# Kernel optimization log

Hardware: AMD Instinct MI355X
Metric: run time of the kernel (lower is better)

The kernel has to match this reference:

```python
import jax, jax.numpy as jnp
import numpy as np

NEG_SLOPE = 0.2

def leaky_relu(x):
    return jnp.where(x >= 0, x, NEG_SLOPE * x)

def conv1x1(x, w, b):
    # x: [n,c,h,w], w: [o,c], b: [o]
    return jnp.einsum('nchw,oc->nohw', x, w) + b[None, :, None, None]

def setup_inputs() -> dict:
    key = jax.random.key(0)
    ks = jax.random.split(key, 7)
    n, c, h, w = 4, 64, 80, 80
    scale = 1.0 / np.sqrt(c)
    return {
        'x': jax.random.normal(ks[0], (n, c, h, w), dtype=jnp.float32),
        'w1': jax.random.normal(ks[1], (c, c), dtype=jnp.float32) * scale,
        'b1': jax.random.normal(ks[2], (c,), dtype=jnp.float32) * 0.01,
        'w2': jax.random.normal(ks[3], (c, c), dtype=jnp.float32) * scale,
        'b2': jax.random.normal(ks[4], (c,), dtype=jnp.float32) * 0.01,
        'w3': jax.random.normal(ks[5], (c, c), dtype=jnp.float32) * scale,
        'b3': jax.random.normal(ks[6], (c,), dtype=jnp.float32) * 0.01,
    }

def reference(x, w1, b1, w2, b2, w3, b3):
    n, c, h, w = x.shape
    e1 = leaky_relu(conv1x1(x, w1, b1))  # [n,c,h,w]
    e2 = leaky_relu(conv1x1(x, w2, b2))
    asm = leaky_relu(conv1x1(x, w3, b3))
    # q: [n, hw, c]; k: [n, c, hw]
    q = e1.transpose(0, 2, 3, 1).reshape(n, h * w, c)
    k = e2.reshape(n, c, h * w)
    score = jax.nn.softmax(jnp.matmul(q, k), axis=2)  # [n, hw, hw]
    v = asm.reshape(n, c, h * w).transpose(0, 2, 1)   # [n, hw, c]
    out = jnp.matmul(score, v)                        # [n, hw, c]
    return out.transpose(0, 2, 1).reshape(n, c, h, w)
```

## Files before the change

kernel.cpp:

```cpp
#include <hip/hip_runtime.h>


typedef __attribute__((ext_vector_type(8))) unsigned short us8;
typedef __attribute__((ext_vector_type(4))) unsigned short us4;
typedef __attribute__((ext_vector_type(8))) __bf16 bf16x8;
typedef __attribute__((ext_vector_type(16))) float f32x16;

#define HW 6400
#define L2E 1.44269504088896340736f
#define KS 5
#define ITERS 20

union V8 { us8 s; us4 h[2]; bf16x8 b; unsigned u4[4]; };

__device__ __forceinline__ unsigned short f32_to_bf16(float f) {
  unsigned u = __float_as_uint(f);
  u += 0x7fffu + ((u >> 16) & 1u);
  return (unsigned short)(u >> 16);
}
__device__ __forceinline__ float bf16_bits_to_f32(unsigned short u) {
  return __uint_as_float(((unsigned)u) << 16);
}
__device__ __forceinline__ unsigned pack_bf16x2(float a, float b) {
#if __has_builtin(__builtin_amdgcn_cvt_pk_bf16_f32)
  auto v = __builtin_amdgcn_cvt_pk_bf16_f32(a, b);
  unsigned u;
  __builtin_memcpy(&u, &v, 4);
  return u;
#else
  unsigned ua = __float_as_uint(a); ua += 0x7fffu + ((ua >> 16) & 1u);
  unsigned ub = __float_as_uint(b); ub += 0x7fffu + ((ub >> 16) & 1u);
  return (ua >> 16) | (ub & 0xffff0000u);
#endif
}

__device__ __forceinline__ void split_hilo(const float* f, V8& hi, V8& lo) {
#pragma unroll
  for (int j = 0; j < 8; ++j) {
    const unsigned short h = f32_to_bf16(f[j]);
    const float r = f[j] - bf16_bits_to_f32(h);
    hi.s[j] = h;
    lo.s[j] = f32_to_bf16(r);
  }
}

__global__ __launch_bounds__(256, 2) void conv_kernel(
    const float* __restrict__ x,
    const float* __restrict__ w1, const float* __restrict__ b1,
    const float* __restrict__ w2, const float* __restrict__ b2,
    const float* __restrict__ w3, const float* __restrict__ b3,
    unsigned short* __restrict__ Qg, unsigned short* __restrict__ Kg,
    unsigned short* __restrict__ Vg) {
  __shared__ __align__(16) float xs[64 * 132];
  __shared__ __align__(16) unsigned short tb[128 * 72];

  const int t = threadIdx.x;
  const int n = blockIdx.y;
  const int p0 = blockIdx.x * 128;
  const int wv = t >> 6;
  const int lane = t & 63;
  const int l31 = lane & 31;
  const int lh = lane >> 5;
  const int ob = (wv & 1) * 32;
  const int pw = (wv >> 1) * 64;

  {
    const int c = t >> 2, qq = t & 3;
    const float* src = x + ((size_t)(n * 64 + c) * HW + p0 + qq * 32);
    float* dst = xs + c * 132 + qq * 32;
#pragma unroll
    for (int i = 0; i < 8; ++i)
      *(float4*)(dst + i * 4) = *(const float4*)(src + i * 4);
  }
  __syncthreads();

  const float* wms[3] = {w1, w2, w3};
  const float* bms[3] = {b1, b2, b3};

#pragma unroll 1
  for (int k = 0; k < 3; ++k) {
    const float* wm = wms[k];
    const float* bm = bms[k];

    V8 ah[4], al[4];
#pragma unroll
    for (int kst = 0; kst < 4; ++kst) {
      const float* wr = wm + (size_t)(ob + l31) * 64 + kst * 16 + lh * 8;
      float wf[8];
      *(float4*)(wf) = *(const float4*)wr;
      *(float4*)(wf + 4) = *(const float4*)(wr + 4);
      split_hilo(wf, ah[kst], al[kst]);
    }

    f32x16 acc[2];
#pragma unroll
    for (int pb = 0; pb < 2; ++pb)
#pragma unroll
      for (int r = 0; r < 16; ++r) acc[pb][r] = 0.f;

#pragma unroll
    for (int kst = 0; kst < 4; ++kst) {
#pragma unroll
      for (int pb = 0; pb < 2; ++pb) {
        float xf[8];
        const float* xp = xs + (kst * 16 + lh * 8) * 132 + pw + pb * 32 + l31;
#pragma unroll
        for (int j = 0; j < 8; ++j) xf[j] = xp[j * 132];
        V8 bh, bl;
        split_hilo(xf, bh, bl);
        acc[pb] = __builtin_amdgcn_mfma_f32_32x32x16_bf16(al[kst].b, bh.b, acc[pb], 0, 0, 0);
        acc[pb] = __builtin_amdgcn_mfma_f32_32x32x16_bf16(ah[kst].b, bl.b, acc[pb], 0, 0, 0);
        acc[pb] = __builtin_amdgcn_mfma_f32_32x32x16_bf16(ah[kst].b, bh.b, acc[pb], 0, 0, 0);
      }
    }

    if (k < 2) {
#pragma unroll
      for (int pb = 0; pb < 2; ++pb) {
#pragma unroll
        for (int rq = 0; rq < 4; ++rq) {
          const int o = ob + 8 * rq + 4 * lh;
          const int pcol = pw + pb * 32 + l31;
          float v[4];
#pragma unroll
          for (int j = 0; j < 4; ++j) {
            float a = acc[pb][4 * rq + j] + bm[o + j];
            a = fmaxf(a, 0.f) + 0.2f * fminf(a, 0.f);
            if (k == 0) a *= L2E;
            v[j] = a;
          }
          unsigned* dst = (unsigned*)(tb + pcol * 72 + o);
          dst[0] = pack_bf16x2(v[0], v[1]);
          dst[1] = pack_bf16x2(v[2], v[3]);
        }
      }
      __syncthreads();
      {
        const int p = t >> 1, half = t & 1;
        const unsigned short* src = tb + p * 72 + half * 32;
        unsigned short* dst = (k == 0 ? Qg : Kg) +
                              (size_t)(n * HW + p0 + p) * 64 + half * 32;
#pragma unroll
        for (int i = 0; i < 4; ++i) *(us8*)(dst + i * 8) = *(const us8*)(src + i * 8);
      }
      __syncthreads();
    } else {
#pragma unroll
      for (int pb = 0; pb < 2; ++pb) {
#pragma unroll
        for (int r = 0; r < 16; ++r) {
          const int o = ob + 8 * (r >> 2) + 4 * lh + (r & 3);
          const int pcol = pw + pb * 32 + l31;
          float a = acc[pb][r] + bm[o];
          a = fmaxf(a, 0.f) + 0.2f * fminf(a, 0.f);
          Vg[(size_t)(n * 64 + o) * HW + p0 + pcol] = f32_to_bf16(a);
        }
      }
    }
  }
}

__global__ __launch_bounds__(256, 4) void attn_kernel(
    const unsigned short* __restrict__ Qg, const unsigned short* __restrict__ Kg,
    const unsigned short* __restrict__ Vg, unsigned short* __restrict__ Opart,
    float* __restrict__ Lpart) {
  __shared__ __align__(16) char smem[36864];
  unsigned short* Otb = (unsigned short*)smem;

  const int t = threadIdx.x;
  const int w = t >> 6;
  const int lane = t & 63;
  const int l31 = lane & 31;
  const int lh = lane >> 5;
  const int nb = blockIdx.y;
  const int qb = blockIdx.x * 128;
  const int ks = blockIdx.z;
  const int key0 = ks * (HW / KS);

  V8 aQ[4];
  {
    const unsigned short* qrow =
        Qg + (size_t)(nb * HW + qb + w * 32 + l31) * 64 + lh * 8;
#pragma unroll
    for (int kst = 0; kst < 4; ++kst) aQ[kst].s = *(const us8*)(qrow + kst * 16);
  }

  f32x16 accO[2];
#pragma unroll
  for (int ci = 0; ci < 2; ++ci)
#pragma unroll
    for (int r = 0; r < 16; ++r) accO[ci][r] = 0.f;
  float lp = 0.f;

  const int soff = (t >> 2) * 72 + (t & 3) * 16;
  const unsigned short* ksrc =
      Kg + (size_t)nb * HW * 64 + (size_t)(key0 + (t >> 2)) * 64 + (t & 3) * 16;
  const unsigned short* vsrc =
      Vg + (size_t)nb * 64 * HW + (size_t)(t >> 2) * HW + key0 + (t & 3) * 16;

  V8 kr0, kr1, vr0, vr1;
  kr0.s = *(const us8*)ksrc;
  kr1.s = *(const us8*)(ksrc + 8);
  vr0.s = *(const us8*)vsrc;
  vr1.s = *(const us8*)(vsrc + 8);
  {
    unsigned short* kd = (unsigned short*)smem + soff;
    unsigned short* vd = (unsigned short*)(smem + 18432) + soff;
    *(us8*)kd = kr0.s; *(us8*)(kd + 8) = kr1.s;
    *(us8*)vd = vr0.s; *(us8*)(vd + 8) = vr1.s;
  }
  __syncthreads();

#pragma unroll 1
  for (int jt = 0; jt < ITERS; ++jt) {
    const int b = jt & 1;
    const unsigned short* Kc = (const unsigned short*)(smem + b * 9216);
    const unsigned short* Vc = (const unsigned short*)(smem + 18432 + b * 9216);
    const bool more = (jt + 1 < ITERS);

    if (more) {
      kr0.s = *(const us8*)(ksrc + (jt + 1) * 4096);
      kr1.s = *(const us8*)(ksrc + (jt + 1) * 4096 + 8);
      vr0.s = *(const us8*)(vsrc + (jt + 1) * 64);
      vr1.s = *(const us8*)(vsrc + (jt + 1) * 64 + 8);
    }

#pragma unroll
    for (int ni = 0; ni < 2; ++ni) {
      V8 ak[4];
#pragma unroll
      for (int kst = 0; kst < 4; ++kst)
        ak[kst].s = *(const us8*)(Kc + (ni * 32 + l31) * 72 + kst * 16 + lh * 8);
      f32x16 sacc;
#pragma unroll
      for (int r = 0; r < 16; ++r) sacc[r] = 0.f;
#pragma unroll
      for (int kst = 0; kst < 4; ++kst)
        sacc = __builtin_amdgcn_mfma_f32_32x32x16_bf16(ak[kst].b, aQ[kst].b,
                                                       sacc, 0, 0, 0);
      uint2 pkg[4];
#pragma unroll
      for (int g = 0; g < 4; ++g) {
        const float p0 = __builtin_amdgcn_exp2f(sacc[4 * g + 0]);
        const float p1 = __builtin_amdgcn_exp2f(sacc[4 * g + 1]);
        const float p2 = __builtin_amdgcn_exp2f(sacc[4 * g + 2]);
        const float p3 = __builtin_amdgcn_exp2f(sacc[4 * g + 3]);
        lp += (p0 + p1) + (p2 + p3);
        pkg[g].x = pack_bf16x2(p0, p1);
        pkg[g].y = pack_bf16x2(p2, p3);
      }

      V8 bv[2][2];
#pragma unroll
      for (int ci = 0; ci < 2; ++ci)
#pragma unroll
        for (int kk = 0; kk < 2; ++kk)
          bv[ci][kk].s = *(const us8*)(Vc + (ci * 32 + l31) * 72 +
                                       (2 * ni + kk) * 16 + lh * 8);
#pragma unroll
      for (int kk = 0; kk < 2; ++kk) {
        const int gb = 2 * kk;
        const uint2 qa = pkg[gb];
        const uint2 qb2 = pkg[gb + 1];
        uint2 send;
        send.x = lh ? qa.x : qb2.x;
        send.y = lh ? qa.y : qb2.y;
        uint2 recv;
        recv.x = __shfl_xor(send.x, 32);
        recv.y = __shfl_xor(send.y, 32);
        const uint2 keep = {lh ? qb2.x : qa.x, lh ? qb2.y : qa.y};
        V8 ap;
        ap.u4[0] = lh ? recv.x : keep.x;
        ap.u4[1] = lh ? recv.y : keep.y;
        ap.u4[2] = lh ? keep.x : recv.x;
        ap.u4[3] = lh ? keep.y : recv.y;
        accO[0] = __builtin_amdgcn_mfma_f32_32x32x16_bf16(ap.b, bv[0][kk].b,
                                                          accO[0], 0, 0, 0);
        accO[1] = __builtin_amdgcn_mfma_f32_32x32x16_bf16(ap.b, bv[1][kk].b,
                                                          accO[1], 0, 0, 0);
      }
    }

    if (more) {
      unsigned short* kd = (unsigned short*)(smem + (1 - b) * 9216) + soff;
      unsigned short* vd = (unsigned short*)(smem + 18432 + (1 - b) * 9216) + soff;
      *(us8*)kd = kr0.s; *(us8*)(kd + 8) = kr1.s;
      *(us8*)vd = vr0.s; *(us8*)(vd + 8) = vr1.s;
      __syncthreads();
    }
  }

  {
    const float lsum = lp + __shfl_xor(lp, 32);
    if (lh == 0)
      Lpart[((size_t)ks * 4 + nb) * HW + qb + w * 32 + l31] = lsum;
  }

  __syncthreads();
#pragma unroll
  for (int ci = 0; ci < 2; ++ci)
#pragma unroll
    for (int r = 0; r < 16; ++r) {
      const int qcol = w * 32 + 8 * (r >> 2) + 4 * lh + (r & 3);
      Otb[(ci * 32 + l31) * 132 + qcol] = f32_to_bf16(accO[ci][r]);
    }
  __syncthreads();
  {
    const int ch = t >> 2, part = t & 3;
    const unsigned short* src = Otb + ch * 132 + part * 32;
    unsigned short* dst =
        Opart + (((size_t)ks * 4 + nb) * 64 + ch) * HW + qb + part * 32;
#pragma unroll
    for (int i = 0; i < 4; ++i) {
      V8 v;
      v.h[0] = *(const us4*)(src + i * 8);
      v.h[1] = *(const us4*)(src + i * 8 + 4);
      *(us8*)(dst + i * 8) = v.s;
    }
  }
}

__global__ __launch_bounds__(256) void combine_kernel(
    const unsigned short* __restrict__ Opart, const float* __restrict__ Lpart,
    float* __restrict__ out) {
  const int tid = blockIdx.x * 256 + threadIdx.x;
  const size_t e = (size_t)tid * 4;
  float4 o = {0.f, 0.f, 0.f, 0.f};
#pragma unroll
  for (int ks = 0; ks < KS; ++ks) {
    const us4 v = *(const us4*)(Opart + (size_t)ks * (4 * 64 * HW) + e);
    o.x += bf16_bits_to_f32(v[0]);
    o.y += bf16_bits_to_f32(v[1]);
    o.z += bf16_bits_to_f32(v[2]);
    o.w += bf16_bits_to_f32(v[3]);
  }
  const int n = (int)(e / (64 * HW));
  const int p = (int)(e % HW);
  float4 l = {0.f, 0.f, 0.f, 0.f};
#pragma unroll
  for (int ks = 0; ks < KS; ++ks) {
    const float4 v = *(const float4*)(Lpart + ((size_t)ks * 4 + n) * HW + p);
    l.x += v.x; l.y += v.y; l.z += v.z; l.w += v.w;
  }
  float4 r;
  r.x = o.x / l.x; r.y = o.y / l.y; r.z = o.z / l.z; r.w = o.w / l.w;
  *(float4*)(out + e) = r;
}

extern "C" void kernel_launch(void* const* d_in, const int* in_sizes, int n_in,
                              void* d_out, int out_size, void* d_ws, size_t ws_size,
                              hipStream_t stream) {
  const float* x = (const float*)d_in[0];
  const float* w1 = (const float*)d_in[1];
  const float* b1 = (const float*)d_in[2];
  const float* w2 = (const float*)d_in[3];
  const float* b2 = (const float*)d_in[4];
  const float* w3 = (const float*)d_in[5];
  const float* b3 = (const float*)d_in[6];
  float* out = (float*)d_out;

  unsigned short* Q = (unsigned short*)d_ws;
  unsigned short* K = Q + (size_t)4 * HW * 64;
  unsigned short* V = K + (size_t)4 * HW * 64;
  unsigned short* Opart = V + (size_t)4 * HW * 64;
  float* Lpart = (float*)(Opart + (size_t)KS * 4 * 64 * HW);

  conv_kernel<<<dim3(50, 4), 256, 0, stream>>>(x, w1, b1, w2, b2, w3, b3,
                                               Q, K, V);
  attn_kernel<<<dim3(50, 4, KS), 256, 0, stream>>>(Q, K, V, Opart, Lpart);
  combine_kernel<<<1600, 256, 0, stream>>>(Opart, Lpart, out);
}
```

Measured before the change: 150.7 us.

## Swizzle K/V shared-memory tiles and use 32x32x8 MFMA for P·V without shuffles

Replaces the padded (stride 72) LDS layout for K and V tiles with an unpadded 128-byte-row layout using an XOR swizzle on 16-byte chunks to avoid bank conflicts. This shrinks shared memory per block. When the 32x32x8 bf16 MFMA builtin exists, the P·V product consumes the softmax accumulator registers directly as 4-element A fragments, removing the cross-half-wave shuffles and selects. That path doubles the number of MFMA issues at half the K depth, and the exact MFMA layout mapping must be correct.

```diff
diff --git a/kernel.cpp b/kernel.cpp
--- a/kernel.cpp
+++ b/kernel.cpp
@@ -4,6 +4,7 @@
 typedef __attribute__((ext_vector_type(8))) unsigned short us8;
 typedef __attribute__((ext_vector_type(4))) unsigned short us4;
 typedef __attribute__((ext_vector_type(8))) __bf16 bf16x8;
+typedef __attribute__((ext_vector_type(4))) short s4;
 typedef __attribute__((ext_vector_type(16))) float f32x16;
 
 #define HW 6400
@@ -12,6 +13,7 @@
 #define ITERS 20
 
 union V8 { us8 s; us4 h[2]; bf16x8 b; unsigned u4[4]; };
+union V4 { us4 h; s4 s; unsigned u2[2]; };
 
 __device__ __forceinline__ unsigned short f32_to_bf16(float f) {
   unsigned u = __float_as_uint(f);
@@ -164,7 +166,7 @@
     const unsigned short* __restrict__ Qg, const unsigned short* __restrict__ Kg,
     const unsigned short* __restrict__ Vg, unsigned short* __restrict__ Opart,
     float* __restrict__ Lpart) {
-  __shared__ __align__(16) char smem[36864];
+  __shared__ __align__(16) char smem[32768];
   unsigned short* Otb = (unsigned short*)smem;
 
   const int t = threadIdx.x;
@@ -185,6 +187,23 @@
     for (int kst = 0; kst < 4; ++kst) aQ[kst].s = *(const us8*)(qrow + kst * 16);
   }
 
+  const int x7 = l31 & 7;
+  int qx[4];
+#pragma unroll
+  for (int kst = 0; kst < 4; ++kst)
+    qx[kst] = l31 * 128 + (((kst * 2 + lh) ^ x7) << 4);
+#if __has_builtin(__builtin_amdgcn_mfma_f32_32x32x8bf16_1k)
+  int qv8[8];
+#pragma unroll
+  for (int m = 0; m < 8; ++m)
+    qv8[m] = l31 * 128 + ((m ^ x7) << 4) + 8 * lh;
+#endif
+
+  const int sr = t >> 2;
+  const int sc0 = 2 * (t & 3);
+  const int so0 = sr * 128 + ((sc0 ^ (sr & 7)) << 4);
+  const int so1 = sr * 128 + (((sc0 + 1) ^ (sr & 7)) << 4);
+
   f32x16 accO[2];
 #pragma unroll
   for (int ci = 0; ci < 2; ++ci)
@@ -192,11 +211,10 @@
     for (int r = 0; r < 16; ++r) accO[ci][r] = 0.f;
   float lp = 0.f;
 
-  const int soff = (t >> 2) * 72 + (t & 3) * 16;
   const unsigned short* ksrc =
-      Kg + (size_t)nb * HW * 64 + (size_t)(key0 + (t >> 2)) * 64 + (t & 3) * 16;
+      Kg + (size_t)nb * HW * 64 + (size_t)(key0 + sr) * 64 + (t & 3) * 16;
   const unsigned short* vsrc =
-      Vg + (size_t)nb * 64 * HW + (size_t)(t >> 2) * HW + key0 + (t & 3) * 16;
+      Vg + (size_t)nb * 64 * HW + (size_t)sr * HW + key0 + (t & 3) * 16;
 
   V8 kr0, kr1, vr0, vr1;
   kr0.s = *(const us8*)ksrc;
@@ -204,18 +222,18 @@
   vr0.s = *(const us8*)vsrc;
   vr1.s = *(const us8*)(vsrc + 8);
   {
-    unsigned short* kd = (unsigned short*)smem + soff;
-    unsigned short* vd = (unsigned short*)(smem + 18432) + soff;
-    *(us8*)kd = kr0.s; *(us8*)(kd + 8) = kr1.s;
-    *(us8*)vd = vr0.s; *(us8*)(vd + 8) = vr1.s;
+    *(us8*)(smem + so0) = kr0.s;
+    *(us8*)(smem + so1) = kr1.s;
+    *(us8*)(smem + 16384 + so0) = vr0.s;
+    *(us8*)(smem + 16384 + so1) = vr1.s;
   }
   __syncthreads();
 
 #pragma unroll 1
   for (int jt = 0; jt < ITERS; ++jt) {
     const int b = jt & 1;
-    const unsigned short* Kc = (const unsigned short*)(smem + b * 9216);
-    const unsigned short* Vc = (const unsigned short*)(smem + 18432 + b * 9216);
+    const char* Kc = smem + b * 8192;
+    const char* Vc = smem + 16384 + b * 8192;
     const bool more = (jt + 1 < ITERS);
 
     if (more) {
@@ -230,7 +248,7 @@
       V8 ak[4];
 #pragma unroll
       for (int kst = 0; kst < 4; ++kst)
-        ak[kst].s = *(const us8*)(Kc + (ni * 32 + l31) * 72 + kst * 16 + lh * 8);
+        ak[kst].s = *(const us8*)(Kc + ni * 4096 + qx[kst]);
       f32x16 sacc;
 #pragma unroll
       for (int r = 0; r < 16; ++r) sacc[r] = 0.f;
@@ -250,13 +268,25 @@
         pkg[g].y = pack_bf16x2(p2, p3);
       }
 
+#if __has_builtin(__builtin_amdgcn_mfma_f32_32x32x8bf16_1k)
+#pragma unroll
+      for (int j8 = 0; j8 < 4; ++j8) {
+        V4 ap;
+        ap.u2[0] = pkg[j8].x;
+        ap.u2[1] = pkg[j8].y;
+        V4 b0, b1;
+        b0.h = *(const us4*)(Vc + qv8[4 * ni + j8]);
+        b1.h = *(const us4*)(Vc + 4096 + qv8[4 * ni + j8]);
+        accO[0] = __builtin_amdgcn_mfma_f32_32x32x8bf16_1k(ap.s, b0.s, accO[0], 0, 0, 0);
+        accO[1] = __builtin_amdgcn_mfma_f32_32x32x8bf16_1k(ap.s, b1.s, accO[1], 0, 0, 0);
+      }
+#else
       V8 bv[2][2];
 #pragma unroll
       for (int ci = 0; ci < 2; ++ci)
 #pragma unroll
         for (int kk = 0; kk < 2; ++kk)
-          bv[ci][kk].s = *(const us8*)(Vc + (ci * 32 + l31) * 72 +
-                                       (2 * ni + kk) * 16 + lh * 8);
+          bv[ci][kk].s = *(const us8*)(Vc + ci * 4096 + qx[2 * ni + kk]);
 #pragma unroll
       for (int kk = 0; kk < 2; ++kk) {
         const int gb = 2 * kk;
@@ -279,13 +309,16 @@
         accO[1] = __builtin_amdgcn_mfma_f32_32x32x16_bf16(ap.b, bv[1][kk].b,
                                                           accO[1], 0, 0, 0);
       }
+#endif
     }
 
     if (more) {
-      unsigned short* kd = (unsigned short*)(smem + (1 - b) * 9216) + soff;
-      unsigned short* vd = (unsigned short*)(smem + 18432 + (1 - b) * 9216) + soff;
-      *(us8*)kd = kr0.s; *(us8*)(kd + 8) = kr1.s;
-      *(us8*)vd = vr0.s; *(us8*)(vd + 8) = vr1.s;
+      char* kd = smem + (1 - b) * 8192;
+      char* vd = smem + 16384 + (1 - b) * 8192;
+      *(us8*)(kd + so0) = kr0.s;
+      *(us8*)(kd + so1) = kr1.s;
+      *(us8*)(vd + so0) = vr0.s;
+      *(us8*)(vd + so1) = vr1.s;
       __syncthreads();
     }
   }
```

Measured after the change: 154.2 us. 2.4% more time.
